# Performance work log

Measured on AMD Instinct MI355X. Metric: run time of the kernel, lower is better.

The kernel has to match this reference:

```python
import jax, jax.numpy as jnp
import numpy as np
import math

B, I, H = 8192, 1024, 1024


def setup_inputs() -> dict:
    key = jax.random.key(0)
    ks = jax.random.split(key, 16)
    stdv = 1.0 / math.sqrt(H)
    u = lambda k, shape: jax.random.uniform(k, shape, jnp.float32, -stdv, stdv)
    inp = {
        'xt': jax.random.normal(ks[0], (B, I), jnp.float32),
        'cx': jax.random.normal(ks[1], (B, H), jnp.float32),
        'hx': jax.random.normal(ks[2], (B, H), jnp.float32),
        'w_fg': u(ks[3], (H, I)), 'w_ig': u(ks[4], (H, I)),
        'w_og': u(ks[5], (H, I)), 'w_ci': u(ks[6], (H, I)),
        'r_fg': u(ks[7], (H, H)), 'r_ig': u(ks[8], (H, H)),
        'r_og': u(ks[9], (H, H)), 'r_ci': u(ks[10], (H, H)),
        'b_fg': u(ks[11], (H,)), 'b_ig': u(ks[12], (H,)),
        'b_og': u(ks[13], (H,)), 'b_ci': u(ks[14], (H,)),
    }
    return inp


def reference(xt, cx, hx, w_fg, w_ig, w_og, w_ci, r_fg, r_ig, r_og, r_ci,
              b_fg, b_ig, b_og, b_ci):
    # Fuse the four input matmuls and four recurrent matmuls into two GEMMs.
    W = jnp.concatenate([w_fg, w_ig, w_og, w_ci], axis=0)  # [4H, I]
    R = jnp.concatenate([r_fg, r_ig, r_og, r_ci], axis=0)  # [4H, H]
    b = jnp.concatenate([b_fg, b_ig, b_og, b_ci], axis=0)  # [4H]
    gates = xt @ W.T + hx @ R.T + b                         # [B, 4H]
    f, i, o, g = jnp.split(gates, 4, axis=-1)
    ft = jax.nn.sigmoid(f)
    it = jax.nn.sigmoid(i)
    ot = jax.nn.sigmoid(o)
    ct = ft * cx + it * jnp.tanh(g)
    ht = ot * jnp.tanh(ct)
    return (ht, ct)
```

## Files before the change

### kernel.cpp

```cpp
#include <hip/hip_runtime.h>

#define B_DIM 8192
#define H_DIM 1024
#define K_DIM 2048
#define N_DIM 4096
#define BH (B_DIM * H_DIM)
#define NT 32
#define TSZ (256 * 64)
#define HALFT (128 * 64)

using frag_ab = __attribute__((ext_vector_type(8))) short;
using frag_cd = __attribute__((ext_vector_type(4))) float;

__device__ __forceinline__ unsigned short f2bf(float f) {
  union { float f; unsigned u; } x; x.f = f;
  return (unsigned short)((x.u + 0x7fffu + ((x.u >> 16) & 1u)) >> 16);
}

__global__ __launch_bounds__(256) void convert_A_kernel(
    const float* __restrict__ xt, const float* __restrict__ hx,
    unsigned short* __restrict__ Ab) {
  int tid = blockIdx.x * 256 + threadIdx.x;
  int flat = tid * 4;
  int m = flat >> 11;
  int k = flat & 2047;
  const float* src = (k < 1024) ? (xt + m * 1024 + k)
                                : (hx + m * 1024 + (k - 1024));
  float4 v = *reinterpret_cast<const float4*>(src);
  ushort4 o;
  o.x = f2bf(v.x); o.y = f2bf(v.y); o.z = f2bf(v.z); o.w = f2bf(v.w);
  *reinterpret_cast<ushort4*>(Ab + flat) = o;
}

__global__ __launch_bounds__(256) void convert_B_kernel(
    const float* __restrict__ w0, const float* __restrict__ w1,
    const float* __restrict__ w2, const float* __restrict__ w3,
    const float* __restrict__ r0, const float* __restrict__ r1,
    const float* __restrict__ r2, const float* __restrict__ r3,
    unsigned short* __restrict__ Bb) {
  int tid = blockIdx.x * 256 + threadIdx.x;
  int flat = tid * 4;
  int n = flat >> 11;
  int k = flat & 2047;
  int tile = n >> 8, c = n & 255;
  int gate = (c >> 4) & 3;
  int h = tile * 64 + ((c >> 6) << 4) + (c & 15);
  const float* wb = (gate == 0) ? w0 : (gate == 1) ? w1 : (gate == 2) ? w2 : w3;
  const float* rb = (gate == 0) ? r0 : (gate == 1) ? r1 : (gate == 2) ? r2 : r3;
  const float* src = (k < 1024) ? (wb + h * 1024 + k)
                                : (rb + h * 1024 + (k - 1024));
  float4 v = *reinterpret_cast<const float4*>(src);
  ushort4 o;
  o.x = f2bf(v.x); o.y = f2bf(v.y); o.z = f2bf(v.z); o.w = f2bf(v.w);
  *reinterpret_cast<ushort4*>(Bb + flat) = o;
}

__device__ __forceinline__ void gload_lds16(const void* g, void* l) {
  __builtin_amdgcn_global_load_lds(
      (const __attribute__((address_space(1))) unsigned int*)g,
      (__attribute__((address_space(3))) unsigned int*)l, 16, 0, 0);
}

__device__ __forceinline__ frag_ab ldsr(const unsigned short* buf, int byteoff) {
  return *reinterpret_cast<const frag_ab*>(
      reinterpret_cast<const char*>(buf) + byteoff);
}

__device__ __forceinline__ float fast_sigmoid(float x) {
  return 1.f / (1.f + __expf(-x));
}
__device__ __forceinline__ float fast_tanh(float x) {
  return 1.f - 2.f / (__expf(2.f * x) + 1.f);
}

#define CBAR asm volatile("" ::: "memory")
#define SBAR do { CBAR; __builtin_amdgcn_s_barrier(); CBAR; } while (0)

#define TILE_BODY(Ac, Bc, Anx, tt, SA, SB, DO_VM4, DO_VM0)                     \
  {                                                                            \
                                              \
    _Pragma("unroll") for (int m = 0; m < 4; ++m)                              \
        Af0[m] = ldsr(Ac, (arow + m * 16) * 128 + c0);                         \
    _Pragma("unroll") for (int n = 0; n < 4; ++n)                              \
        Bf0[n] = ldsr(Bc, (brow + n * 16) * 128 + c0);                         \
    SBAR;                                                                      \
    __builtin_amdgcn_s_setprio(1);                                             \
    _Pragma("unroll") for (int m = 0; m < 4; ++m)                              \
        _Pragma("unroll") for (int n = 0; n < 4; ++n)                          \
            acc[m][n] = __builtin_amdgcn_mfma_f32_16x16x32_bf16(               \
                Af0[m], Bf0[n], acc[m][n], 0, 0, 0);                           \
    __builtin_amdgcn_s_setprio(0);                                             \
                          \
    _Pragma("unroll") for (int m = 0; m < 4; ++m)                              \
        Af1[m] = ldsr(Ac, (arow + m * 16) * 128 + c1);                         \
    _Pragma("unroll") for (int n = 0; n < 4; ++n)                              \
        Bf1[n] = ldsr(Bc, (brow + n * 16) * 128 + c1);                         \
    if (SA) {                                                                  \
      stage(Ag + (size_t)((tt) + 1) * 64, (Anx));                              \
      stage(Ag + (size_t)((tt) + 1) * 64 + 128 * K_DIM, (Anx) + HALFT);        \
    }                                                                          \
    SBAR;                                                                      \
    __builtin_amdgcn_s_setprio(1);                                             \
    _Pragma("unroll") for (int m = 0; m < 4; ++m)                              \
        _Pragma("unroll") for (int n = 0; n < 4; ++n)                          \
            acc[m][n] = __builtin_amdgcn_mfma_f32_16x16x32_bf16(               \
                Af1[m], Bf1[n], acc[m][n], 0, 0, 0);                           \
    __builtin_amdgcn_s_setprio(0);                                             \
             \
    _Pragma("unroll") for (int m = 0; m < 4; ++m)                              \
        Af0[m] = ldsr(Ac, (arow + 64 + m * 16) * 128 + c0);                    \
    if (SB) stage(Bg + (size_t)((tt) + 2) * 64, (Bc));                         \
    SBAR;                                                                      \
    __builtin_amdgcn_s_setprio(1);                                             \
    _Pragma("unroll") for (int m = 0; m < 4; ++m)                              \
        _Pragma("unroll") for (int n = 0; n < 4; ++n)                          \
            acc[4 + m][n] = __builtin_amdgcn_mfma_f32_16x16x32_bf16(           \
                Af0[m], Bf0[n], acc[4 + m][n], 0, 0, 0);                       \
    __builtin_amdgcn_s_setprio(0);                                             \
                   \
    _Pragma("unroll") for (int m = 0; m < 4; ++m)                              \
        Af1[m] = ldsr(Ac, (arow + 64 + m * 16) * 128 + c1);                    \
    if (SB) stage(Bg + (size_t)((tt) + 2) * 64 + 128 * K_DIM, (Bc) + HALFT);   \
    SBAR;                                                                      \
    __builtin_amdgcn_s_setprio(1);                                             \
    _Pragma("unroll") for (int m = 0; m < 4; ++m)                              \
        _Pragma("unroll") for (int n = 0; n < 4; ++n)                          \
            acc[4 + m][n] = __builtin_amdgcn_mfma_f32_16x16x32_bf16(           \
                Af1[m], Bf1[n], acc[4 + m][n], 0, 0, 0);                       \
    __builtin_amdgcn_s_setprio(0);                                             \
    if (DO_VM4) asm volatile("s_waitcnt vmcnt(4)" ::: "memory");               \
    if (DO_VM0) asm volatile("s_waitcnt vmcnt(0)" ::: "memory");               \
  }

__global__ __launch_bounds__(512, 2) void lstm_gemm_kernel(
    const unsigned short* __restrict__ Ab,
    const unsigned short* __restrict__ Bb,
    const float* __restrict__ cx,
    const float* __restrict__ b_f, const float* __restrict__ b_i,
    const float* __restrict__ b_o, const float* __restrict__ b_g,
    float* __restrict__ out) {
  extern __shared__ unsigned short smem[];
  unsigned short* const As0 = smem;
  unsigned short* const As1 = smem + TSZ;
  unsigned short* const Bs0 = smem + 2 * TSZ;
  unsigned short* const Bs1 = smem + 3 * TSZ;

  const int bid = blockIdx.x;
  const int swz = (bid & 7) * 64 + (bid >> 3);
  const int bm = swz >> 4;
  const int bn = swz & 15;

  const int tid = threadIdx.x;
  const int lane = tid & 63;
  const int wid = tid >> 6;
  const int wr = wid >> 2, wc = wid & 3;
  const int ln = lane & 15, kh = lane >> 4;

  const unsigned short* Ag = Ab + (size_t)(bm * 256) * K_DIM;
  const unsigned short* Bg = Bb + (size_t)(bn * 256) * K_DIM;

  const int srow = wid * 16 + (lane >> 3);
  const size_t gs0 = (size_t)srow * K_DIM + (((lane & 7) ^ (lane >> 3)) << 3);
  const size_t gs1 = gs0 + (size_t)8 * K_DIM;
  const int ld0 = wid * 2048 + lane * 16;
  const int ld1 = ld0 + 1024;
  auto stage = [&](const unsigned short* g, unsigned short* l) {
    gload_lds16(g + gs0, reinterpret_cast<char*>(l) + ld0);
    gload_lds16(g + gs1, reinterpret_cast<char*>(l) + ld1);
  };

  const int inv = (ln & 7) << 4;
  const int c0 = (kh * 16) ^ inv;
  const int c1 = (64 + kh * 16) ^ inv;
  const int arow = wr * 128 + ln;
  const int brow = wc * 64 + ln;

  frag_cd acc[8][4] = {};
  frag_ab Af0[4], Af1[4], Bf0[4], Bf1[4];

  stage(Ag, As0);
  stage(Ag + 128 * K_DIM, As0 + HALFT);
  stage(Bg, Bs0);
  stage(Bg + 128 * K_DIM, Bs0 + HALFT);
  stage(Bg + 64, Bs1);
  stage(Bg + 64 + 128 * K_DIM, Bs1 + HALFT);
  asm volatile("s_waitcnt vmcnt(4)" ::: "memory");
  SBAR;

  for (int u = 0; u < 15; ++u) {
    const int e = 2 * u;
    TILE_BODY(As0, Bs0, As1, e, 1, 1, 1, 0);
    TILE_BODY(As1, Bs1, As0, e + 1, 1, 1, 1, 0);
  }
  TILE_BODY(As0, Bs0, As1, 30, 1, 0, 0, 1);
  TILE_BODY(As1, Bs1, As0, 31, 0, 0, 0, 0);

  const int hcol = bn * 64 + wc * 16 + ln;
  const float bfv = b_f[hcol], biv = b_i[hcol], bov = b_o[hcol], bgv = b_g[hcol];
  const int row_base = bm * 256 + wr * 128 + kh * 4;
#pragma unroll
  for (int mi = 0; mi < 8; ++mi) {
#pragma unroll
    for (int j = 0; j < 4; ++j) {
      const int row = row_base + mi * 16 + j;
      float fp = acc[mi][0][j] + bfv;
      float ip = acc[mi][1][j] + biv;
      float op = acc[mi][2][j] + bov;
      float gp = acc[mi][3][j] + bgv;
      float ft = fast_sigmoid(fp);
      float it = fast_sigmoid(ip);
      float ot = fast_sigmoid(op);
      float gt = fast_tanh(gp);
      float cold = cx[(size_t)row * H_DIM + hcol];
      float ct = ft * cold + it * gt;
      float ht = ot * fast_tanh(ct);
      out[(size_t)row * H_DIM + hcol] = ht;
      out[BH + (size_t)row * H_DIM + hcol] = ct;
    }
  }
}

extern "C" void kernel_launch(void* const* d_in, const int* in_sizes, int n_in,
                              void* d_out, int out_size, void* d_ws, size_t ws_size,
                              hipStream_t stream) {
  const float* xt   = (const float*)d_in[0];
  const float* cxp  = (const float*)d_in[1];
  const float* hx   = (const float*)d_in[2];
  const float* w_fg = (const float*)d_in[3];
  const float* w_ig = (const float*)d_in[4];
  const float* w_og = (const float*)d_in[5];
  const float* w_ci = (const float*)d_in[6];
  const float* r_fg = (const float*)d_in[7];
  const float* r_ig = (const float*)d_in[8];
  const float* r_og = (const float*)d_in[9];
  const float* r_ci = (const float*)d_in[10];
  const float* b_fg = (const float*)d_in[11];
  const float* b_ig = (const float*)d_in[12];
  const float* b_og = (const float*)d_in[13];
  const float* b_ci = (const float*)d_in[14];

  unsigned short* Abf = (unsigned short*)d_ws;
  unsigned short* Bbf = Abf + (size_t)B_DIM * K_DIM;
  float* out = (float*)d_out;

  convert_A_kernel<<<dim3(B_DIM * K_DIM / 4 / 256), dim3(256), 0, stream>>>(
      xt, hx, Abf);
  convert_B_kernel<<<dim3(N_DIM * K_DIM / 4 / 256), dim3(256), 0, stream>>>(
      w_fg, w_ig, w_og, w_ci, r_fg, r_ig, r_og, r_ci, Bbf);
  lstm_gemm_kernel<<<dim3((B_DIM / 256) * (N_DIM / 256)), dim3(512),
                     131072, stream>>>(
      Abf, Bbf, cxp, b_fg, b_ig, b_og, b_ci, out);
}
```

Before: 158.3 us.

## Software-pipeline LDS fragment reads across tiles and spread global staging

Restructures the GEMM main loop so the first fragments of the next tile are read from LDS at the end of the current tile, overlapping those reads with the preceding MFMA phase. Global-to-LDS staging for A and B is split across the four phases. The wait is moved before the third phase and loosened to vmcnt(2). Scheduling barriers pin instruction order. The aim is to hide LDS read latency and smooth memory traffic, at the cost of more live registers and tighter correctness reasoning about buffer reuse and wait counts.

After: 157.9 us. No clear change (-0.3%).

```diff
diff --git a/kernel.cpp b/kernel.cpp
--- a/kernel.cpp
+++ b/kernel.cpp
@@ -75,61 +75,66 @@
 
 #define CBAR asm volatile("" ::: "memory")
 #define SBAR do { CBAR; __builtin_amdgcn_s_barrier(); CBAR; } while (0)
-
-#define TILE_BODY(Ac, Bc, Anx, tt, SA, SB, DO_VM4, DO_VM0)                     \
+#define SCHED0 __builtin_amdgcn_sched_barrier(0)
+
+#define TILE_BODY(Ac, Bc, An, Bn, tt, SA, SB, VM2, VM0, RD)                    \
   {                                                                            \
-                                              \
-    _Pragma("unroll") for (int m = 0; m < 4; ++m)                              \
-        Af0[m] = ldsr(Ac, (arow + m * 16) * 128 + c0);                         \
-    _Pragma("unroll") for (int n = 0; n < 4; ++n)                              \
-        Bf0[n] = ldsr(Bc, (brow + n * 16) * 128 + c0);                         \
-    SBAR;                                                                      \
-    __builtin_amdgcn_s_setprio(1);                                             \
-    _Pragma("unroll") for (int m = 0; m < 4; ++m)                              \
-        _Pragma("unroll") for (int n = 0; n < 4; ++n)                          \
-            acc[m][n] = __builtin_amdgcn_mfma_f32_16x16x32_bf16(               \
-                Af0[m], Bf0[n], acc[m][n], 0, 0, 0);                           \
-    __builtin_amdgcn_s_setprio(0);                                             \
-                          \
-    _Pragma("unroll") for (int m = 0; m < 4; ++m)                              \
-        Af1[m] = ldsr(Ac, (arow + m * 16) * 128 + c1);                         \
+                                                             \
+    _Pragma("unroll") for (int m = 0; m < 4; ++m)                              \
+        AfB[m] = ldsr(Ac, (arow + m * 16) * 128 + c1);                         \
     _Pragma("unroll") for (int n = 0; n < 4; ++n)                              \
         Bf1[n] = ldsr(Bc, (brow + n * 16) * 128 + c1);                         \
-    if (SA) {                                                                  \
-      stage(Ag + (size_t)((tt) + 1) * 64, (Anx));                              \
-      stage(Ag + (size_t)((tt) + 1) * 64 + 128 * K_DIM, (Anx) + HALFT);        \
+    if (SA) stage(Ag + (size_t)((tt) + 1) * 64, (An));                         \
+    SCHED0;                                                                    \
+    SBAR;                                                                      \
+    __builtin_amdgcn_s_setprio(1);                                             \
+    _Pragma("unroll") for (int m = 0; m < 4; ++m)                              \
+        _Pragma("unroll") for (int n = 0; n < 4; ++n)                          \
+            acc[m][n] = __builtin_amdgcn_mfma_f32_16x16x32_bf16(               \
+                AfA[m], Bf0[n], acc[m][n], 0, 0, 0);                           \
+    __builtin_amdgcn_s_setprio(0);                                             \
+                                                             \
+    _Pragma("unroll") for (int m = 0; m < 4; ++m)                              \
+        AfA[m] = ldsr(Ac, (arow + 64 + m * 16) * 128 + c0);                    \
+    if (SA) stage(Ag + (size_t)((tt) + 1) * 64 + 128 * K_DIM, (An) + HALFT);   \
+    SCHED0;                                                                    \
+    SBAR;                                                                      \
+    __builtin_amdgcn_s_setprio(1);                                             \
+    _Pragma("unroll") for (int m = 0; m < 4; ++m)                              \
+        _Pragma("unroll") for (int n = 0; n < 4; ++n)                          \
+            acc[m][n] = __builtin_amdgcn_mfma_f32_16x16x32_bf16(               \
+                AfB[m], Bf1[n], acc[m][n], 0, 0, 0);                           \
+    __builtin_amdgcn_s_setprio(0);                                             \
+                        \
+    _Pragma("unroll") for (int m = 0; m < 4; ++m)                              \
+        AfB[m] = ldsr(Ac, (arow + 64 + m * 16) * 128 + c1);                    \
+    if (SB) stage(Bg + (size_t)((tt) + 2) * 64, (Bc));                         \
+    if (VM2) asm volatile("s_waitcnt vmcnt(2)" ::: "memory");                  \
+    if (VM0) asm volatile("s_waitcnt vmcnt(0)" ::: "memory");                  \
+    SCHED0;                                                                    \
+    SBAR;                                                                      \
+    __builtin_amdgcn_s_setprio(1);                                             \
+    _Pragma("unroll") for (int m = 0; m < 4; ++m)                              \
+        _Pragma("unroll") for (int n = 0; n < 4; ++n)                          \
+            acc[4 + m][n] = __builtin_amdgcn_mfma_f32_16x16x32_bf16(           \
+                AfA[m], Bf0[n], acc[4 + m][n], 0, 0, 0);                       \
+    __builtin_amdgcn_s_setprio(0);                                             \
+                                 \
+    if (RD) {                                                                  \
+      _Pragma("unroll") for (int m = 0; m < 4; ++m)                            \
+          AfA[m] = ldsr(An, (arow + m * 16) * 128 + c0);                       \
+      _Pragma("unroll") for (int n = 0; n < 4; ++n)                            \
+          Bf0[n] = ldsr(Bn, (brow + n * 16) * 128 + c0);                       \
     }                                                                          \
-    SBAR;                                                                      \
-    __builtin_amdgcn_s_setprio(1);                                             \
-    _Pragma("unroll") for (int m = 0; m < 4; ++m)                              \
-        _Pragma("unroll") for (int n = 0; n < 4; ++n)                          \
-            acc[m][n] = __builtin_amdgcn_mfma_f32_16x16x32_bf16(               \
-                Af1[m], Bf1[n], acc[m][n], 0, 0, 0);                           \
-    __builtin_amdgcn_s_setprio(0);                                             \
-             \
-    _Pragma("unroll") for (int m = 0; m < 4; ++m)                              \
-        Af0[m] = ldsr(Ac, (arow + 64 + m * 16) * 128 + c0);                    \
-    if (SB) stage(Bg + (size_t)((tt) + 2) * 64, (Bc));                         \
+    if (SB) stage(Bg + (size_t)((tt) + 2) * 64 + 128 * K_DIM, (Bc) + HALFT);   \
+    SCHED0;                                                                    \
     SBAR;                                                                      \
     __builtin_amdgcn_s_setprio(1);                                             \
     _Pragma("unroll") for (int m = 0; m < 4; ++m)                              \
         _Pragma("unroll") for (int n = 0; n < 4; ++n)                          \
             acc[4 + m][n] = __builtin_amdgcn_mfma_f32_16x16x32_bf16(           \
-                Af0[m], Bf0[n], acc[4 + m][n], 0, 0, 0);                       \
-    __builtin_amdgcn_s_setprio(0);                                             \
-                   \
-    _Pragma("unroll") for (int m = 0; m < 4; ++m)                              \
-        Af1[m] = ldsr(Ac, (arow + 64 + m * 16) * 128 + c1);                    \
-    if (SB) stage(Bg + (size_t)((tt) + 2) * 64 + 128 * K_DIM, (Bc) + HALFT);   \
-    SBAR;                                                                      \
-    __builtin_amdgcn_s_setprio(1);                                             \
-    _Pragma("unroll") for (int m = 0; m < 4; ++m)                              \
-        _Pragma("unroll") for (int n = 0; n < 4; ++n)                          \
-            acc[4 + m][n] = __builtin_amdgcn_mfma_f32_16x16x32_bf16(           \
-                Af1[m], Bf1[n], acc[4 + m][n], 0, 0, 0);                       \
-    __builtin_amdgcn_s_setprio(0);                                             \
-    if (DO_VM4) asm volatile("s_waitcnt vmcnt(4)" ::: "memory");               \
-    if (DO_VM0) asm volatile("s_waitcnt vmcnt(0)" ::: "memory");               \
+                AfB[m], Bf1[n], acc[4 + m][n], 0, 0, 0);                       \
+    __builtin_amdgcn_s_setprio(0);                                             \
   }
 
 __global__ __launch_bounds__(512, 2) void lstm_gemm_kernel(
@@ -176,7 +181,7 @@
   const int brow = wc * 64 + ln;
 
   frag_cd acc[8][4] = {};
-  frag_ab Af0[4], Af1[4], Bf0[4], Bf1[4];
+  frag_ab AfA[4], AfB[4], Bf0[4], Bf1[4];
 
   stage(Ag, As0);
   stage(Ag + 128 * K_DIM, As0 + HALFT);
@@ -186,14 +191,20 @@
   stage(Bg + 64 + 128 * K_DIM, Bs1 + HALFT);
   asm volatile("s_waitcnt vmcnt(4)" ::: "memory");
   SBAR;
+#pragma unroll
+  for (int m = 0; m < 4; ++m)
+    AfA[m] = ldsr(As0, (arow + m * 16) * 128 + c0);
+#pragma unroll
+  for (int n = 0; n < 4; ++n)
+    Bf0[n] = ldsr(Bs0, (brow + n * 16) * 128 + c0);
 
   for (int u = 0; u < 15; ++u) {
     const int e = 2 * u;
-    TILE_BODY(As0, Bs0, As1, e, 1, 1, 1, 0);
-    TILE_BODY(As1, Bs1, As0, e + 1, 1, 1, 1, 0);
+    TILE_BODY(As0, Bs0, As1, Bs1, e, 1, 1, 1, 0, 1);
+    TILE_BODY(As1, Bs1, As0, Bs0, e + 1, 1, 1, 1, 0, 1);
   }
-  TILE_BODY(As0, Bs0, As1, 30, 1, 0, 0, 1);
-  TILE_BODY(As1, Bs1, As0, 31, 0, 0, 0, 0);
+  TILE_BODY(As0, Bs0, As1, Bs1, 30, 1, 0, 0, 1, 1);
+  TILE_BODY(As1, Bs1, As0, Bs0, 31, 0, 0, 0, 0, 0);
 
   const int hcol = bn * 64 + wc * 16 + ln;
   const float bfv = b_f[hcol], biv = b_i[hcol], bov = b_o[hcol], bgv = b_g[hcol];
```

## Restructure LDS fragment loads to hold both K halves and split by N quadrant

Applied to the files above, without the earlier changes.

Rewrites the inner tile schedule so each wave loads both K halves (c0,c1) of its A and B fragments at once, then issues MFMAs over N sub-blocks of two columns instead of K halves. It adds explicit lgkmcnt waits, a sched_barrier, and extra barriers after each MFMA phase, and it spreads the global-to-LDS stage calls differently across the four phases. The aim is to interleave LDS reads, global staging and MFMA more evenly and so hide LDS latency. The cost is more barriers per tile and a different register footprint for the fragment arrays.

After: 159.3 us. About the same (+0.6%).

```diff
diff --git a/kernel.cpp b/kernel.cpp
--- a/kernel.cpp
+++ b/kernel.cpp
@@ -75,61 +75,74 @@
 
 #define CBAR asm volatile("" ::: "memory")
 #define SBAR do { CBAR; __builtin_amdgcn_s_barrier(); CBAR; } while (0)
-
-#define TILE_BODY(Ac, Bc, Anx, tt, SA, SB, DO_VM4, DO_VM0)                     \
+#define LGKM0 do { asm volatile("s_waitcnt lgkmcnt(0)" ::: "memory");          \
+                   __builtin_amdgcn_sched_barrier(0); } while (0)
+#define LGKM8 asm volatile("s_waitcnt lgkmcnt(8)" ::: "memory")
+
+#define TILE_BODY(Ac, Bc, Anx, tt, SA, SB, VM4, VM0)                           \
   {                                                                            \
-                                              \
-    _Pragma("unroll") for (int m = 0; m < 4; ++m)                              \
-        Af0[m] = ldsr(Ac, (arow + m * 16) * 128 + c0);                         \
-    _Pragma("unroll") for (int n = 0; n < 4; ++n)                              \
-        Bf0[n] = ldsr(Bc, (brow + n * 16) * 128 + c0);                         \
-    SBAR;                                                                      \
-    __builtin_amdgcn_s_setprio(1);                                             \
-    _Pragma("unroll") for (int m = 0; m < 4; ++m)                              \
-        _Pragma("unroll") for (int n = 0; n < 4; ++n)                          \
-            acc[m][n] = __builtin_amdgcn_mfma_f32_16x16x32_bf16(               \
-                Af0[m], Bf0[n], acc[m][n], 0, 0, 0);                           \
-    __builtin_amdgcn_s_setprio(0);                                             \
+             \
+    _Pragma("unroll") for (int m = 0; m < 4; ++m)                              \
+        _Pragma("unroll") for (int k = 0; k < 2; ++k)                          \
+            Afr[m][k] = ldsr(Ac, (arow + m * 16) * 128 + (k ? c1 : c0));       \
+    _Pragma("unroll") for (int n = 0; n < 2; ++n)                              \
+        _Pragma("unroll") for (int k = 0; k < 2; ++k)                          \
+            Bfr[n][k] = ldsr(Bc, (brow + n * 16) * 128 + (k ? c1 : c0));       \
+    if (SA) stage(Ag + (size_t)((tt) + 1) * 64, (Anx));                        \
+    LGKM8;                                                                     \
+    SBAR;                                                                      \
+    LGKM0;                                                                     \
+    __builtin_amdgcn_s_setprio(1);                                             \
+    _Pragma("unroll") for (int m = 0; m < 4; ++m)                              \
+        _Pragma("unroll") for (int n = 0; n < 2; ++n)                          \
+            _Pragma("unroll") for (int k = 0; k < 2; ++k)                      \
+                acc[m][n] = __builtin_amdgcn_mfma_f32_16x16x32_bf16(           \
+                    Afr[m][k], Bfr[n][k], acc[m][n], 0, 0, 0);                 \
+    __builtin_amdgcn_s_setprio(0);                                             \
+    SBAR;                                                                      \
                           \
-    _Pragma("unroll") for (int m = 0; m < 4; ++m)                              \
-        Af1[m] = ldsr(Ac, (arow + m * 16) * 128 + c1);                         \
-    _Pragma("unroll") for (int n = 0; n < 4; ++n)                              \
-        Bf1[n] = ldsr(Bc, (brow + n * 16) * 128 + c1);                         \
-    if (SA) {                                                                  \
-      stage(Ag + (size_t)((tt) + 1) * 64, (Anx));                              \
-      stage(Ag + (size_t)((tt) + 1) * 64 + 128 * K_DIM, (Anx) + HALFT);        \
-    }                                                                          \
-    SBAR;                                                                      \
-    __builtin_amdgcn_s_setprio(1);                                             \
-    _Pragma("unroll") for (int m = 0; m < 4; ++m)                              \
-        _Pragma("unroll") for (int n = 0; n < 4; ++n)                          \
-            acc[m][n] = __builtin_amdgcn_mfma_f32_16x16x32_bf16(               \
-                Af1[m], Bf1[n], acc[m][n], 0, 0, 0);                           \
-    __builtin_amdgcn_s_setprio(0);                                             \
-             \
-    _Pragma("unroll") for (int m = 0; m < 4; ++m)                              \
-        Af0[m] = ldsr(Ac, (arow + 64 + m * 16) * 128 + c0);                    \
+    _Pragma("unroll") for (int n = 2; n < 4; ++n)                              \
+        _Pragma("unroll") for (int k = 0; k < 2; ++k)                          \
+            Bfr[n][k] = ldsr(Bc, (brow + n * 16) * 128 + (k ? c1 : c0));       \
+    if (SA) stage(Ag + (size_t)((tt) + 1) * 64 + 128 * K_DIM, (Anx) + HALFT);  \
+    SBAR;                                                                      \
+    LGKM0;                                                                     \
+    __builtin_amdgcn_s_setprio(1);                                             \
+    _Pragma("unroll") for (int m = 0; m < 4; ++m)                              \
+        _Pragma("unroll") for (int n = 2; n < 4; ++n)                          \
+            _Pragma("unroll") for (int k = 0; k < 2; ++k)                      \
+                acc[m][n] = __builtin_amdgcn_mfma_f32_16x16x32_bf16(           \
+                    Afr[m][k], Bfr[n][k], acc[m][n], 0, 0, 0);                 \
+    __builtin_amdgcn_s_setprio(0);                                             \
+    SBAR;                                                                      \
+          \
+    _Pragma("unroll") for (int m = 0; m < 4; ++m)                              \
+        _Pragma("unroll") for (int k = 0; k < 2; ++k)                          \
+            Afr[m][k] = ldsr(Ac, (arow + 64 + m * 16) * 128 + (k ? c1 : c0));  \
     if (SB) stage(Bg + (size_t)((tt) + 2) * 64, (Bc));                         \
     SBAR;                                                                      \
-    __builtin_amdgcn_s_setprio(1);                                             \
-    _Pragma("unroll") for (int m = 0; m < 4; ++m)                              \
-        _Pragma("unroll") for (int n = 0; n < 4; ++n)                          \
-            acc[4 + m][n] = __builtin_amdgcn_mfma_f32_16x16x32_bf16(           \
-                Af0[m], Bf0[n], acc[4 + m][n], 0, 0, 0);                       \
-    __builtin_amdgcn_s_setprio(0);                                             \
-                   \
-    _Pragma("unroll") for (int m = 0; m < 4; ++m)                              \
-        Af1[m] = ldsr(Ac, (arow + 64 + m * 16) * 128 + c1);                    \
+    LGKM0;                                                                     \
+    __builtin_amdgcn_s_setprio(1);                                             \
+    _Pragma("unroll") for (int m = 0; m < 4; ++m)                              \
+        _Pragma("unroll") for (int n = 0; n < 2; ++n)                          \
+            _Pragma("unroll") for (int k = 0; k < 2; ++k)                      \
+                acc[4 + m][n] = __builtin_amdgcn_mfma_f32_16x16x32_bf16(       \
+                    Afr[m][k], Bfr[n][k], acc[4 + m][n], 0, 0, 0);             \
+    __builtin_amdgcn_s_setprio(0);                                             \
+    SBAR;                                                                      \
+     \
     if (SB) stage(Bg + (size_t)((tt) + 2) * 64 + 128 * K_DIM, (Bc) + HALFT);   \
-    SBAR;                                                                      \
-    __builtin_amdgcn_s_setprio(1);                                             \
-    _Pragma("unroll") for (int m = 0; m < 4; ++m)                              \
-        _Pragma("unroll") for (int n = 0; n < 4; ++n)                          \
-            acc[4 + m][n] = __builtin_amdgcn_mfma_f32_16x16x32_bf16(           \
-                Af1[m], Bf1[n], acc[4 + m][n], 0, 0, 0);                       \
-    __builtin_amdgcn_s_setprio(0);                                             \
-    if (DO_VM4) asm volatile("s_waitcnt vmcnt(4)" ::: "memory");               \
-    if (DO_VM0) asm volatile("s_waitcnt vmcnt(0)" ::: "memory");               \
+    if (VM4) asm volatile("s_waitcnt vmcnt(4)" ::: "memory");                  \
+    if (VM0) asm volatile("s_waitcnt vmcnt(0)" ::: "memory");                  \
+    SBAR;                                                                      \
+    __builtin_amdgcn_s_setprio(1);                                             \
+    _Pragma("unroll") for (int m = 0; m < 4; ++m)                              \
+        _Pragma("unroll") for (int n = 2; n < 4; ++n)                          \
+            _Pragma("unroll") for (int k = 0; k < 2; ++k)                      \
+                acc[4 + m][n] = __builtin_amdgcn_mfma_f32_16x16x32_bf16(       \
+                    Afr[m][k], Bfr[n][k], acc[4 + m][n], 0, 0, 0);             \
+    __builtin_amdgcn_s_setprio(0);                                             \
+    SBAR;                                                                      \
   }
 
 __global__ __launch_bounds__(512, 2) void lstm_gemm_kernel(
@@ -176,7 +189,7 @@
   const int brow = wc * 64 + ln;
 
   frag_cd acc[8][4] = {};
-  frag_ab Af0[4], Af1[4], Bf0[4], Bf1[4];
+  frag_ab Afr[4][2], Bfr[4][2];
 
   stage(Ag, As0);
   stage(Ag + 128 * K_DIM, As0 + HALFT);
```
